# Kernel optimization log

Measured on AMD Instinct MI355X. Metric: run time of the kernel, lower is better.

## Reference

```python
import jax, jax.numpy as jnp
import numpy as np

HIDDEN = 4096
N_HEADS = 32
N_KV_HEADS = 8
HEAD_DIM = HIDDEN // N_HEADS  # 128
Q_SIZE = N_HEADS * HEAD_DIM
KV_SIZE = N_KV_HEADS * HEAD_DIM
ROPE_THETA = 10000.0
EPS = 1e-5
SCALE = HEAD_DIM ** -0.5


def _headwise_layernorm(x, weight, eps):
    # x: [B,S,H,D], weight: [H,D]; LayerNorm over last dim (head_dim), fp32 math
    xf = x.astype(jnp.float32)
    mean = xf.mean(-1, keepdims=True)
    var = jnp.square(xf - mean).mean(-1, keepdims=True)
    y = (xf - mean) * jax.lax.rsqrt(var + eps)
    return (weight.astype(jnp.float32) * y).astype(x.dtype)


def _rope_gptj(x, positions):
    # non-neox (GPT-J) style: rotate interleaved pairs. x: [B,S,H,D]
    half = HEAD_DIM // 2
    inv_freq = 1.0 / (ROPE_THETA ** (jnp.arange(0, HEAD_DIM, 2, dtype=jnp.float32) / HEAD_DIM))
    ang = positions.astype(jnp.float32)[..., None] * inv_freq  # [B,S,half]
    cos = jnp.cos(ang)[:, :, None, :]  # [B,S,1,half]
    sin = jnp.sin(ang)[:, :, None, :]
    x1 = x[..., 0::2]
    x2 = x[..., 1::2]
    o1 = x1 * cos - x2 * sin
    o2 = x2 * cos + x1 * sin
    # re-interleave
    out = jnp.stack([o1, o2], axis=-1).reshape(x.shape)
    return out.astype(x.dtype)


def setup_inputs() -> dict:
    key = jax.random.key(0)
    k1, k2, k3, k4 = jax.random.split(key, 4)
    B, S = 2, 2048
    positions = jnp.tile(jnp.arange(S, dtype=jnp.int32)[None, :], (B, 1))
    hidden_states = jax.random.normal(k1, (B, S, HIDDEN), dtype=jnp.float32)
    Wqkv = jax.random.normal(k2, (HIDDEN, Q_SIZE + 2 * KV_SIZE), dtype=jnp.float32) * (HIDDEN ** -0.5)
    Wo = jax.random.normal(k3, (Q_SIZE, HIDDEN), dtype=jnp.float32) * (Q_SIZE ** -0.5)
    kq, kk = jax.random.split(k4)
    q_norm_w = jnp.ones((N_HEADS, HEAD_DIM), jnp.float32) + 0.02 * jax.random.normal(kq, (N_HEADS, HEAD_DIM))
    k_norm_w = jnp.ones((N_KV_HEADS, HEAD_DIM), jnp.float32) + 0.02 * jax.random.normal(kk, (N_KV_HEADS, HEAD_DIM))
    return {"positions": positions, "hidden_states": hidden_states, "Wqkv": Wqkv,
            "q_norm_w": q_norm_w, "k_norm_w": k_norm_w, "Wo": Wo}


def reference(positions, hidden_states, Wqkv, q_norm_w, k_norm_w, Wo):
    B, S, _ = hidden_states.shape
    qkv = hidden_states @ Wqkv  # [B,S,Q+2KV]
    q, k, v = jnp.split(qkv, [Q_SIZE, Q_SIZE + KV_SIZE], axis=-1)
    q = q.reshape(B, S, N_HEADS, HEAD_DIM)
    k = k.reshape(B, S, N_KV_HEADS, HEAD_DIM)
    v = v.reshape(B, S, N_KV_HEADS, HEAD_DIM)
    # per-head qk-norm
    q = _headwise_layernorm(q, q_norm_w, EPS)
    k = _headwise_layernorm(k, k_norm_w, EPS)
    # non-neox RoPE
    q = _rope_gptj(q, positions)
    k = _rope_gptj(k, positions)
    # GQA: repeat kv heads
    n_rep = N_HEADS // N_KV_HEADS
    k = jnp.repeat(k, n_rep, axis=2)  # [B,S,H,D]
    v = jnp.repeat(v, n_rep, axis=2)
    scores = jnp.einsum('bqhd,bkhd->bhqk', q, k) * SCALE
    causal = jnp.tril(jnp.ones((S, S), dtype=bool))
    scores = jnp.where(causal[None, None], scores, jnp.finfo(scores.dtype).min)
    probs = jax.nn.softmax(scores, axis=-1)
    attn = jnp.einsum('bhqk,bkhd->bqhd', probs, v).reshape(B, S, Q_SIZE)
    return attn @ Wo
```

## Files before the change

### kernel.cpp

```cpp
#include <hip/hip_runtime.h>
#include <hip/hip_bf16.h>
#include <cstdint>

typedef unsigned short u16;
typedef unsigned int u32;
typedef __attribute__((ext_vector_type(8))) short bf16x8;
typedef __attribute__((ext_vector_type(4))) float f32x4;
typedef __attribute__((ext_vector_type(16))) float f32x16;
typedef __attribute__((ext_vector_type(4))) unsigned int u32x4;

#define HIDDEN 4096
#define NH 32
#define NKV 8
#define HD 128
#define QSZ 4096
#define KVSZ 1024
#define QKV_N 6144
#define SEQ 2048
#define NB 2
#define NTOK (NB*SEQ)
#define ATT_SCALE 0.08838834764831845f
#define LOG2E 1.4426950408889634f
#define LN_EPS 1e-5f
#define THRD 12.0f

__device__ __forceinline__ u16 f2bf(float f) {
  union { float f; u32 u; } a; a.f = f;
  u32 r = a.u + 0x7fffu + ((a.u >> 16) & 1u);
  return (u16)(r >> 16);
}
__device__ __forceinline__ float bf2f(u16 h) {
  union { u32 u; float f; } a; a.u = ((u32)h) << 16;
  return a.f;
}

__device__ __forceinline__ void gload_lds16(const void* g, void* l) {
  __builtin_amdgcn_global_load_lds(
      (const __attribute__((address_space(1))) void*)g,
      (__attribute__((address_space(3))) void*)l,
      16, 0, 0);
}

__global__ __launch_bounds__(256)
void conv_f32_bf16(const float* __restrict__ in, u16* __restrict__ out, int n8) {
  int i = blockIdx.x * 256 + threadIdx.x;
  if (i >= n8) return;
  const float4* p = (const float4*)in + (size_t)i * 2;
  float4 v0 = p[0], v1 = p[1];
  u32x4 o;
  o.x = (u32)f2bf(v0.x) | ((u32)f2bf(v0.y) << 16);
  o.y = (u32)f2bf(v0.z) | ((u32)f2bf(v0.w) << 16);
  o.z = (u32)f2bf(v1.x) | ((u32)f2bf(v1.y) << 16);
  o.w = (u32)f2bf(v1.z) | ((u32)f2bf(v1.w) << 16);
  ((u32x4*)out)[i] = o;
}

__global__ __launch_bounds__(256)
void transp_f32_bf16(const float* __restrict__ in, u16* __restrict__ out, int R, int C) {
  __shared__ float tile[32][33];
  int c0 = blockIdx.x << 5, r0 = blockIdx.y << 5;
  int tx = threadIdx.x & 31, ty = threadIdx.x >> 5;
  #pragma unroll
  for (int j = 0; j < 32; j += 8)
    tile[ty + j][tx] = in[(long)(r0 + ty + j) * C + c0 + tx];
  __syncthreads();
  #pragma unroll
  for (int j = 0; j < 32; j += 8)
    out[(long)(c0 + ty + j) * R + r0 + tx] = f2bf(tile[tx][ty + j]);
}

template<typename OutT>
__global__ __launch_bounds__(512, 4)
void gemm_bt9(const u16* __restrict__ A, const u16* __restrict__ Bt,
              OutT* __restrict__ C, int N, int K) {
  extern __shared__ char smem[];
  const int t = threadIdx.x;
  const int lane = t & 63, w = t >> 6;
  const int wr = w >> 2, wc = w & 3;
  const int l31 = lane & 31, g2 = lane >> 5;
  const int bm = blockIdx.y, bn = blockIdx.x;

  const u16* pA;  const u16* pB0;  const u16* pB1;
  {
    int ci = t;
    int line = ci >> 3, phys = ci & 7;
    int lg = phys ^ (line & 7);
    pA = A + (long)(bm * 128 + 2 * line + (lg >> 2)) * K + ((lg & 3) << 3);
    ci = t;
    line = ci >> 3; phys = ci & 7; lg = phys ^ (line & 7);
    pB0 = Bt + (long)(bn * 256 + 2 * line + (lg >> 2)) * K + ((lg & 3) << 3);
    ci = t + 512;
    line = ci >> 3; phys = ci & 7; lg = phys ^ (line & 7);
    pB1 = Bt + (long)(bn * 256 + 2 * line + (lg >> 2)) * K + ((lg & 3) << 3);
  }
  const int dS = w * 1024;

  const int lhalf = l31 >> 1;
  const int lgbase = (l31 & 1) * 4 + g2;

  f32x16 acc[2][2];
  #pragma unroll
  for (int i = 0; i < 2; ++i)
    #pragma unroll
    for (int j = 0; j < 2; ++j)
      #pragma unroll
      for (int r = 0; r < 16; ++r) acc[i][j][r] = 0.f;

  const int nt = K >> 5;
  char* cbase = smem;
  char* nbase = smem + 24576;
  char* sbase = smem + 49152;

  #define STAGE9(dst, koff) { \
    gload_lds16(pA  + (koff), (dst) + dS); \
    gload_lds16(pB0 + (koff), (dst) + 8192 + dS); \
    gload_lds16(pB1 + (koff), (dst) + 16384 + dS); }

  STAGE9(cbase, 0);
  STAGE9(nbase, 32);
  asm volatile("s_waitcnt vmcnt(3)" ::: "memory");
  __builtin_amdgcn_s_barrier();
  __builtin_amdgcn_sched_barrier(0);

  #define READ9(dst, s) { \
    const int lg_ = lgbase + (s) * 2; \
    { int ln_ = wr * 32 + lhalf;          int ph_ = lg_ ^ (ln_ & 7); \
      dst[0] = *(const bf16x8*)(cbase + ln_ * 128 + ph_ * 16); } \
    { int ln_ = wr * 32 + 16 + lhalf;     int ph_ = lg_ ^ (ln_ & 7); \
      dst[1] = *(const bf16x8*)(cbase + ln_ * 128 + ph_ * 16); } \
    { int ln_ = wc * 32 + lhalf;          int ph_ = lg_ ^ (ln_ & 7); \
      dst[2] = *(const bf16x8*)(cbase + 8192 + ln_ * 128 + ph_ * 16); } \
    { int ln_ = wc * 32 + 16 + lhalf;     int ph_ = lg_ ^ (ln_ & 7); \
      dst[3] = *(const bf16x8*)(cbase + 8192 + ln_ * 128 + ph_ * 16); } }
  #define MFMA9(f) { \
    __builtin_amdgcn_s_setprio(1); \
    acc[0][0] = __builtin_amdgcn_mfma_f32_32x32x16_bf16(f[0], f[2], acc[0][0], 0, 0, 0); \
    acc[0][1] = __builtin_amdgcn_mfma_f32_32x32x16_bf16(f[0], f[3], acc[0][1], 0, 0, 0); \
    acc[1][0] = __builtin_amdgcn_mfma_f32_32x32x16_bf16(f[1], f[2], acc[1][0], 0, 0, 0); \
    acc[1][1] = __builtin_amdgcn_mfma_f32_32x32x16_bf16(f[1], f[3], acc[1][1], 0, 0, 0); \
    __builtin_amdgcn_s_setprio(0); }

  for (int tt = 0; tt < nt; ++tt) {
    const long sk = (long)((tt + 2 < nt) ? (tt + 2) : (nt - 1)) * 32;
    bf16x8 f0[4], f1[4];
    READ9(f0, 0);
    READ9(f1, 1);
    STAGE9(sbase, sk);
    MFMA9(f0);
    MFMA9(f1);
    asm volatile("s_waitcnt vmcnt(3)" ::: "memory");
    __builtin_amdgcn_s_barrier();
    __builtin_amdgcn_sched_barrier(0);
    char* tmp = cbase; cbase = nbase; nbase = sbase; sbase = tmp;
  }
  #undef READ9
  #undef MFMA9
  #undef STAGE9

  #pragma unroll
  for (int mf = 0; mf < 2; ++mf)
    #pragma unroll
    for (int nf = 0; nf < 2; ++nf)
      #pragma unroll
      for (int r = 0; r < 16; ++r) {
        long row = bm * 128 + wr * 64 + mf * 32 + (r & 3) + 8 * (r >> 2) + 4 * g2;
        long col = bn * 256 + wc * 64 + nf * 32 + l31;
        float v = acc[mf][nf][r];
        if constexpr (sizeof(OutT) == 2) C[row * N + col] = f2bf(v);
        else                             C[row * N + col] = v;
      }
}

__device__ __forceinline__ void ln_rope_head(const u16* __restrict__ src,
                                             const float* __restrict__ wgt,
                                             u16* __restrict__ dst,
                                             int lane, float sa, float ca, float scale) {
  u32 xr = *(const u32*)(src + 2 * lane);
  float x1 = bf2f((u16)(xr & 0xffffu)), x2 = bf2f((u16)(xr >> 16));
  float ssum = x1 + x2;
  #pragma unroll
  for (int off = 1; off < 64; off <<= 1) ssum += __shfl_xor(ssum, off);
  float mean = ssum * (1.0f / 128.0f);
  float e1 = x1 - mean, e2 = x2 - mean;
  float vv = e1 * e1 + e2 * e2;
  #pragma unroll
  for (int off = 1; off < 64; off <<= 1) vv += __shfl_xor(vv, off);
  float rstd = rsqrtf(vv * (1.0f / 128.0f) + LN_EPS);
  float y1 = e1 * rstd * wgt[2 * lane];
  float y2 = e2 * rstd * wgt[2 * lane + 1];
  float o1 = (y1 * ca - y2 * sa) * scale;
  float o2 = (y2 * ca + y1 * sa) * scale;
  *(u32*)(dst + 2 * lane) = (u32)f2bf(o1) | ((u32)f2bf(o2) << 16);
}

__global__ __launch_bounds__(512)
void ln_rope(const u16* __restrict__ qkv, const int* __restrict__ pos,
             const float* __restrict__ qw, const float* __restrict__ kw,
             u16* __restrict__ qo, u16* __restrict__ ko) {
  const int s = blockIdx.x, b = blockIdx.y;
  const int t = threadIdx.x, lane = t & 63, w = t >> 6;
  const long base = (long)(b * SEQ + s) * QKV_N;
  const int p = pos[b * SEQ + s];
  const float expo = (float)(2 * lane) * (1.0f / 128.0f);
  const float inv_freq = exp2f(-expo * 13.287712379549449f);
  float sa, ca;
  sincosf((float)p * inv_freq, &sa, &ca);
  #pragma unroll
  for (int hh = 0; hh < 4; ++hh) {
    int h = w + hh * 8;
    ln_rope_head(qkv + base + h * HD, qw + h * HD,
                 qo + (((long)b * NH + h) * SEQ + s) * HD, lane, sa, ca,
                 ATT_SCALE * LOG2E);
  }
  ln_rope_head(qkv + base + QSZ + w * HD, kw + w * HD,
               ko + (((long)b * NKV + w) * SEQ + s) * HD, lane, sa, ca, 1.0f);
}

__global__ __launch_bounds__(256)
void v_transp(const u16* __restrict__ qkv, u16* __restrict__ vt) {
  __shared__ u16 tile[32][33];
  int s0 = blockIdx.x * 32, d0 = blockIdx.y * 32;
  int bk = blockIdx.z;
  int b = bk >> 3, kvh = bk & 7;
  int tx = threadIdx.x & 31, ty = threadIdx.x >> 5;
  const u16* src = qkv + ((long)(b * SEQ) + s0) * QKV_N + QSZ + KVSZ + kvh * HD + d0;
  #pragma unroll
  for (int j = 0; j < 32; j += 8)
    tile[ty + j][tx] = src[(long)(ty + j) * QKV_N + tx];
  __syncthreads();
  u16* dst = vt + (((long)bk) * HD + d0) * SEQ + s0;
  #pragma unroll
  for (int j = 0; j < 32; j += 8)
    dst[(long)(ty + j) * SEQ + tx] = tile[tx][ty + j];
}

__global__ __launch_bounds__(512, 2)
void flash_attn3(const u16* __restrict__ Qg, const u16* __restrict__ Kg,
                 const u16* __restrict__ Vtg, u16* __restrict__ Og) {
  const int lin = blockIdx.x;
  const int b = lin >> 7;
  const int rem = lin & 127;
  const int h = rem >> 2;
  const int qp = rem & 3;
  const int kvh = h >> 2;
  const int t = threadIdx.x, lane = t & 63, w = t >> 6;
  const int hh = lane >> 5, l31 = lane & 31;

  __shared__ u16 Klds[2][64 * 128];
  __shared__ u16 Vlds[2][128 * 64];

  const u16* Kbase = Kg + ((long)b * NKV + kvh) * (long)SEQ * HD;
  const u16* Vtbase = Vtg + ((long)b * NKV + kvh) * (long)HD * SEQ;

  auto STAGE = [&](int buf, int kt) {
    const int kv0 = kt * 64;
    #pragma unroll
    for (int i = 0; i < 2; ++i) {
      int c = t + i * 512;
      int kv = c >> 4, cc = c & 15;
      int cl = (cc & 8) | ((cc ^ kv) & 7);
      gload_lds16(Kbase + (long)(kv0 + kv) * HD + cl * 8,
                  (char*)(&Klds[buf][0]) + (i * 512 + w * 64) * 16);
    }
    #pragma unroll
    for (int i = 0; i < 2; ++i) {
      int c = t + i * 512;
      int d = c >> 3, cc = c & 7;
      int cl = cc ^ (d & 7);
      gload_lds16(Vtbase + (long)d * SEQ + kv0 + cl * 8,
                  (char*)(&Vlds[buf][0]) + (i * 512 + w * 64) * 16);
    }
  };

  for (int seg = 0; seg < 2; ++seg) {
    const int qt = seg ? qp : (7 - qp);
    const int wq0 = qt * 256 + w * 32;
    const int q = wq0 + l31;
    const u16* Qbase = Qg + (((long)b * NH + h) * SEQ + q) * HD + hh * 8;
    bf16x8 qf[8];
    #pragma unroll
    for (int ks = 0; ks < 8; ++ks) qf[ks] = *(const bf16x8*)(Qbase + ks * 16);

    f32x16 o[4];
    #pragma unroll
    for (int i = 0; i < 4; ++i)
      #pragma unroll
      for (int r = 0; r < 16; ++r) o[i][r] = 0.f;
    float m = -1e30f, l = 0.f;
    const int nt = qt * 4 + 4;

    __syncthreads();
    STAGE(0, 0);
    __syncthreads();
    int cur = 0;
    for (int kt = 0; kt < nt; ++kt) {
      const int kv0 = kt * 64;
      if (kt + 1 < nt) STAGE(cur ^ 1, kt + 1);
      if (kv0 <= wq0 + 31) {
        const char* Kb = (const char*)(&Klds[cur][0]);
        const char* Vb = (const char*)(&Vlds[cur][0]);
        f32x16 st[2];
        #pragma unroll
        for (int tt = 0; tt < 2; ++tt)
          #pragma unroll
          for (int r = 0; r < 16; ++r) st[tt][r] = 0.f;
        __builtin_amdgcn_s_setprio(1);
        #pragma unroll
        for (int tt = 0; tt < 2; ++tt) {
          if (kv0 + tt * 32 <= wq0 + 31) {
            #pragma unroll
            for (int ks = 0; ks < 8; ++ks) {
              int ch = ks * 2 + hh;
              int pc = (ch & 8) | ((ch ^ l31) & 7);
              bf16x8 kf = *(const bf16x8*)(Kb + (tt * 32 + l31) * 256 + pc * 16);
              st[tt] = __builtin_amdgcn_mfma_f32_32x32x16_bf16(kf, qf[ks], st[tt], 0, 0, 0);
            }
          }
        }
        __builtin_amdgcn_s_setprio(0);
        if (kv0 + 63 > wq0) {
          #pragma unroll
          for (int tt = 0; tt < 2; ++tt)
            #pragma unroll
            for (int r = 0; r < 16; ++r) {
              int kva = kv0 + tt * 32 + (r & 3) + 8 * (r >> 2) + 4 * hh;
              if (kva > q) st[tt][r] = -1e30f;
            }
        }
        float p0 = -1e30f, p1 = -1e30f, p2 = -1e30f, p3 = -1e30f;
        #pragma unroll
        for (int tt = 0; tt < 2; ++tt)
          #pragma unroll
          for (int r = 0; r < 16; r += 4) {
            p0 = fmaxf(p0, st[tt][r]);
            p1 = fmaxf(p1, st[tt][r + 1]);
            p2 = fmaxf(p2, st[tt][r + 2]);
            p3 = fmaxf(p3, st[tt][r + 3]);
          }
        float mx = fmaxf(fmaxf(p0, p1), fmaxf(p2, p3));
        mx = fmaxf(mx, __shfl_xor(mx, 32));
        if (!__all(mx - m <= THRD)) {
          float mn = fmaxf(m, mx);
          float sc = exp2f(m - mn);
          m = mn;
          float scr[16];
          #pragma unroll
          for (int r = 0; r < 16; ++r)
            scr[r] = __shfl(sc, (r & 3) + 8 * (r >> 2) + 4 * hh);
          #pragma unroll
          for (int db = 0; db < 4; ++db)
            #pragma unroll
            for (int r = 0; r < 16; ++r) o[db][r] *= scr[r];
          l *= sc;
        }
        float s0 = 0.f, s1 = 0.f, s2 = 0.f, s3 = 0.f;
        #pragma unroll
        for (int tt = 0; tt < 2; ++tt)
          #pragma unroll
          for (int r = 0; r < 16; r += 4) {
            float e0 = exp2f(st[tt][r] - m);
            float e1 = exp2f(st[tt][r + 1] - m);
            float e2 = exp2f(st[tt][r + 2] - m);
            float e3 = exp2f(st[tt][r + 3] - m);
            st[tt][r] = e0; st[tt][r + 1] = e1; st[tt][r + 2] = e2; st[tt][r + 3] = e3;
            s0 += e0; s1 += e1; s2 += e2; s3 += e3;
          }
        float rs = (s0 + s1) + (s2 + s3);
        rs += __shfl_xor(rs, 32);
        l += rs;
        bf16x8 pa[4];
        #pragma unroll
        for (int k4 = 0; k4 < 4; ++k4) {
          int s8 = (k4 & 1) * 8, tt = k4 >> 1;
          u32 x0 = (u32)f2bf(st[tt][s8 + 0]) | ((u32)f2bf(st[tt][s8 + 1]) << 16);
          u32 x1 = (u32)f2bf(st[tt][s8 + 2]) | ((u32)f2bf(st[tt][s8 + 3]) << 16);
          u32 y0 = (u32)f2bf(st[tt][s8 + 4]) | ((u32)f2bf(st[tt][s8 + 5]) << 16);
          u32 y1 = (u32)f2bf(st[tt][s8 + 6]) | ((u32)f2bf(st[tt][s8 + 7]) << 16);
          u32 x0s = (u32)__shfl_xor((int)x0, 32), x1s = (u32)__shfl_xor((int)x1, 32);
          u32 y0s = (u32)__shfl_xor((int)y0, 32), y1s = (u32)__shfl_xor((int)y1, 32);
          union { u32 u[4]; bf16x8 v; } pk;
          pk.u[0] = hh ? y0s : x0;
          pk.u[1] = hh ? y1s : x1;
          pk.u[2] = hh ? y0 : x0s;
          pk.u[3] = hh ? y1 : x1s;
          pa[k4] = pk.v;
        }
        __builtin_amdgcn_s_setprio(1);
        #pragma unroll
        for (int k4 = 0; k4 < 4; ++k4)
          #pragma unroll
          for (int db = 0; db < 4; ++db) {
            int ch = k4 * 2 + hh;
            int pcc = ch ^ (l31 & 7);
            bf16x8 vf = *(const bf16x8*)(Vb + (db * 32 + l31) * 128 + pcc * 16);
            o[db] = __builtin_amdgcn_mfma_f32_32x32x16_bf16(pa[k4], vf, o[db], 0, 0, 0);
          }
        __builtin_amdgcn_s_setprio(0);
      }
      __syncthreads();
      cur ^= 1;
    }
    float linv = 1.0f / l;
    float li[16];
    #pragma unroll
    for (int r = 0; r < 16; ++r)
      li[r] = __shfl(linv, (r & 3) + 8 * (r >> 2) + 4 * hh);
    #pragma unroll
    for (int db = 0; db < 4; ++db)
      #pragma unroll
      for (int r = 0; r < 16; ++r) {
        int qr = wq0 + (r & 3) + 8 * (r >> 2) + 4 * hh;
        Og[((long)b * SEQ + qr) * QSZ + h * HD + db * 32 + l31] = f2bf(o[db][r] * li[r]);
      }
  }
}

extern "C" void kernel_launch(void* const* d_in, const int* in_sizes, int n_in,
                              void* d_out, int out_size, void* d_ws, size_t ws_size,
                              hipStream_t stream) {
  const int*   positions = (const int*)d_in[0];
  const float* hidden    = (const float*)d_in[1];
  const float* Wqkv      = (const float*)d_in[2];
  const float* qnw       = (const float*)d_in[3];
  const float* knw       = (const float*)d_in[4];
  const float* Wo        = (const float*)d_in[5];
  float* out = (float*)d_out;
  char* ws = (char*)d_ws;
  const size_t MB = 1024 * 1024;
  u16* hbf   = (u16*)(ws + 0);
  u16* WqkvT = (u16*)(ws + 32 * MB);
  u16* qkvb  = (u16*)(ws + 80 * MB);
  u16* q_arr = (u16*)(ws + 0);
  u16* k_arr = (u16*)(ws + 32 * MB);
  u16* vt_arr= (u16*)(ws + 40 * MB);
  u16* WoT   = (u16*)(ws + 48 * MB);
  u16* Oarr  = (u16*)(ws + 80 * MB);

  const int GEMM_LDS = 3 * 24576;
  (void)hipFuncSetAttribute((const void*)&gemm_bt9<u16>,
        hipFuncAttributeMaxDynamicSharedMemorySize, GEMM_LDS);
  (void)hipFuncSetAttribute((const void*)&gemm_bt9<float>,
        hipFuncAttributeMaxDynamicSharedMemorySize, GEMM_LDS);

  conv_f32_bf16<<<dim3(NTOK * HIDDEN / 8 / 256), 256, 0, stream>>>(hidden, hbf, NTOK * HIDDEN / 8);
  transp_f32_bf16<<<dim3(QKV_N / 32, HIDDEN / 32), 256, 0, stream>>>(Wqkv, WqkvT, HIDDEN, QKV_N);
  gemm_bt9<u16><<<dim3(QKV_N / 256, NTOK / 128), 512, GEMM_LDS, stream>>>(hbf, WqkvT, qkvb, QKV_N, HIDDEN);
  ln_rope<<<dim3(SEQ, NB), 512, 0, stream>>>(qkvb, positions, qnw, knw, q_arr, k_arr);
  v_transp<<<dim3(SEQ / 32, HD / 32, NB * NKV), 256, 0, stream>>>(qkvb, vt_arr);
  transp_f32_bf16<<<dim3(HIDDEN / 32, QSZ / 32), 256, 0, stream>>>(Wo, WoT, QSZ, HIDDEN);
  flash_attn3<<<dim3(256), 512, 0, stream>>>(q_arr, k_arr, vt_arr, Oarr);
  gemm_bt9<float><<<dim3(HIDDEN / 256, NTOK / 128), 512, GEMM_LDS, stream>>>(Oarr, WoT, out, HIDDEN, QSZ);
}
```

Baseline: 598.6 us.

## Use 256x256 double-buffered GEMM tile with 64-deep K for output projection

```diff
diff --git a/kernel.cpp b/kernel.cpp
--- a/kernel.cpp
+++ b/kernel.cpp
@@ -164,6 +164,113 @@
       #pragma unroll
       for (int r = 0; r < 16; ++r) {
         long row = bm * 128 + wr * 64 + mf * 32 + (r & 3) + 8 * (r >> 2) + 4 * g2;
+        long col = bn * 256 + wc * 64 + nf * 32 + l31;
+        float v = acc[mf][nf][r];
+        if constexpr (sizeof(OutT) == 2) C[row * N + col] = f2bf(v);
+        else                             C[row * N + col] = v;
+      }
+}
+
+template<typename OutT>
+__global__ __launch_bounds__(512, 2)
+void gemm_bt4(const u16* __restrict__ A, const u16* __restrict__ Bt,
+              OutT* __restrict__ C, int N, int K) {
+  extern __shared__ char smem[];
+  const int t = threadIdx.x;
+  const int lane = t & 63, w = t >> 6;
+  const int wr = w >> 2, wc = w & 3;
+  const int l31 = lane & 31, g2 = lane >> 5;
+  const int bm = blockIdx.y, bn = blockIdx.x;
+
+  const u16* pA[4]; const u16* pB[4];
+  int dS[4];
+  #pragma unroll
+  for (int i = 0; i < 4; ++i) {
+    int ci = t + i * 512;
+    int row = ci >> 3;
+    int c = (ci & 7) ^ (row & 7);
+    pA[i] = A  + (long)(bm * 256 + row) * K + (c << 3);
+    pB[i] = Bt + (long)(bn * 256 + row) * K + (c << 3);
+    dS[i] = (i * 512 + w * 64) * 16;
+  }
+
+  const int arowB = (wr * 128 + l31) * 128;
+  const int browB = 32768 + (wc * 64 + l31) * 128;
+
+  f32x16 acc[4][2];
+  #pragma unroll
+  for (int i = 0; i < 4; ++i)
+    #pragma unroll
+    for (int j = 0; j < 2; ++j)
+      #pragma unroll
+      for (int r = 0; r < 16; ++r) acc[i][j][r] = 0.f;
+
+  const int nt = K >> 6;
+  char* cb = smem;
+  char* sb = smem + 65536;
+
+  #pragma unroll
+  for (int i = 0; i < 4; ++i) gload_lds16(pA[i], cb + dS[i]);
+  #pragma unroll
+  for (int i = 0; i < 4; ++i) gload_lds16(pB[i], cb + 32768 + dS[i]);
+  asm volatile("s_waitcnt vmcnt(0)" ::: "memory");
+  __builtin_amdgcn_s_barrier();
+  __builtin_amdgcn_sched_barrier(0);
+
+  #define READ_KK4(dst, kkv) { \
+    const int pcb = ((((kkv) * 2 + g2)) ^ (l31 & 7)) << 4; \
+    dst[0] = *(const bf16x8*)(cb + arowB + pcb); \
+    dst[1] = *(const bf16x8*)(cb + arowB + 4096 + pcb); \
+    dst[2] = *(const bf16x8*)(cb + arowB + 8192 + pcb); \
+    dst[3] = *(const bf16x8*)(cb + arowB + 12288 + pcb); \
+    dst[4] = *(const bf16x8*)(cb + browB + pcb); \
+    dst[5] = *(const bf16x8*)(cb + browB + 4096 + pcb); }
+  #define MFMA_KK4(f) { \
+    __builtin_amdgcn_s_setprio(1); \
+    acc[0][0] = __builtin_amdgcn_mfma_f32_32x32x16_bf16(f[0], f[4], acc[0][0], 0, 0, 0); \
+    acc[0][1] = __builtin_amdgcn_mfma_f32_32x32x16_bf16(f[0], f[5], acc[0][1], 0, 0, 0); \
+    acc[1][0] = __builtin_amdgcn_mfma_f32_32x32x16_bf16(f[1], f[4], acc[1][0], 0, 0, 0); \
+    acc[1][1] = __builtin_amdgcn_mfma_f32_32x32x16_bf16(f[1], f[5], acc[1][1], 0, 0, 0); \
+    acc[2][0] = __builtin_amdgcn_mfma_f32_32x32x16_bf16(f[2], f[4], acc[2][0], 0, 0, 0); \
+    acc[2][1] = __builtin_amdgcn_mfma_f32_32x32x16_bf16(f[2], f[5], acc[2][1], 0, 0, 0); \
+    acc[3][0] = __builtin_amdgcn_mfma_f32_32x32x16_bf16(f[3], f[4], acc[3][0], 0, 0, 0); \
+    acc[3][1] = __builtin_amdgcn_mfma_f32_32x32x16_bf16(f[3], f[5], acc[3][1], 0, 0, 0); \
+    __builtin_amdgcn_s_setprio(0); }
+
+  for (int tt = 0; tt < nt; ++tt) {
+    const long sk = (long)((tt + 1 < nt) ? (tt + 1) : (nt - 1)) * 64;
+    bf16x8 f0[6], f1[6];
+    READ_KK4(f0, 0);
+    gload_lds16(pA[0] + sk, sb + dS[0]);
+    gload_lds16(pA[1] + sk, sb + dS[1]);
+    READ_KK4(f1, 1);
+    gload_lds16(pA[2] + sk, sb + dS[2]);
+    gload_lds16(pA[3] + sk, sb + dS[3]);
+    MFMA_KK4(f0);
+    gload_lds16(pB[0] + sk, sb + 32768 + dS[0]);
+    gload_lds16(pB[1] + sk, sb + 32768 + dS[1]);
+    MFMA_KK4(f1);
+    READ_KK4(f0, 2);
+    gload_lds16(pB[2] + sk, sb + 32768 + dS[2]);
+    gload_lds16(pB[3] + sk, sb + 32768 + dS[3]);
+    MFMA_KK4(f0);
+    READ_KK4(f1, 3);
+    MFMA_KK4(f1);
+    asm volatile("s_waitcnt vmcnt(0)" ::: "memory");
+    __builtin_amdgcn_s_barrier();
+    __builtin_amdgcn_sched_barrier(0);
+    char* tmp = cb; cb = sb; sb = tmp;
+  }
+  #undef READ_KK4
+  #undef MFMA_KK4
+
+  #pragma unroll
+  for (int mf = 0; mf < 4; ++mf)
+    #pragma unroll
+    for (int nf = 0; nf < 2; ++nf)
+      #pragma unroll
+      for (int r = 0; r < 16; ++r) {
+        long row = bm * 256 + wr * 128 + mf * 32 + (r & 3) + 8 * (r >> 2) + 4 * g2;
         long col = bn * 256 + wc * 64 + nf * 32 + l31;
         float v = acc[mf][nf][r];
         if constexpr (sizeof(OutT) == 2) C[row * N + col] = f2bf(v);
@@ -436,18 +543,19 @@
   u16* WoT   = (u16*)(ws + 48 * MB);
   u16* Oarr  = (u16*)(ws + 80 * MB);
 
-  const int GEMM_LDS = 3 * 24576;
+  const int GEMM9_LDS = 3 * 24576;
+  const int GEMM4_LDS = 2 * 65536;
   (void)hipFuncSetAttribute((const void*)&gemm_bt9<u16>,
-        hipFuncAttributeMaxDynamicSharedMemorySize, GEMM_LDS);
-  (void)hipFuncSetAttribute((const void*)&gemm_bt9<float>,
-        hipFuncAttributeMaxDynamicSharedMemorySize, GEMM_LDS);
+        hipFuncAttributeMaxDynamicSharedMemorySize, GEMM9_LDS);
+  (void)hipFuncSetAttribute((const void*)&gemm_bt4<float>,
+        hipFuncAttributeMaxDynamicSharedMemorySize, GEMM4_LDS);
 
   conv_f32_bf16<<<dim3(NTOK * HIDDEN / 8 / 256), 256, 0, stream>>>(hidden, hbf, NTOK * HIDDEN / 8);
   transp_f32_bf16<<<dim3(QKV_N / 32, HIDDEN / 32), 256, 0, stream>>>(Wqkv, WqkvT, HIDDEN, QKV_N);
-  gemm_bt9<u16><<<dim3(QKV_N / 256, NTOK / 128), 512, GEMM_LDS, stream>>>(hbf, WqkvT, qkvb, QKV_N, HIDDEN);
+  gemm_bt9<u16><<<dim3(QKV_N / 256, NTOK / 128), 512, GEMM9_LDS, stream>>>(hbf, WqkvT, qkvb, QKV_N, HIDDEN);
   ln_rope<<<dim3(SEQ, NB), 512, 0, stream>>>(qkvb, positions, qnw, knw, q_arr, k_arr);
   v_transp<<<dim3(SEQ / 32, HD / 32, NB * NKV), 256, 0, stream>>>(qkvb, vt_arr);
   transp_f32_bf16<<<dim3(HIDDEN / 32, QSZ / 32), 256, 0, stream>>>(Wo, WoT, QSZ, HIDDEN);
   flash_attn3<<<dim3(256), 512, 0, stream>>>(q_arr, k_arr, vt_arr, Oarr);
-  gemm_bt9<float><<<dim3(HIDDEN / 256, NTOK / 128), 512, GEMM_LDS, stream>>>(Oarr, WoT, out, HIDDEN, QSZ);
-}
+  gemm_bt4<float><<<dim3(HIDDEN / 256, NTOK / 256), 512, GEMM4_LDS, stream>>>(Oarr, WoT, out, HIDDEN, QSZ);
+}
```

Measured after the change: 578.5 us. -3.4%, faster.
